# Kernel optimization log

Hardware: AMD Instinct MI355X
Metric: run time of the kernel (lower is better)

Reference implementation:

```python
import jax, jax.numpy as jnp
import numpy as np

N, E, G = 20000, 600000, 128
NF, HID, L, H = 16, 128, 4, 4
C = HID // H  # 32 per-head out dim
BN_EPS = 1e-5


def setup_inputs() -> dict:
    key = jax.random.key(0)
    ks = jax.random.split(key, 24)
    inp = {}
    inp['x'] = jax.random.normal(ks[0], (N, NF), dtype=jnp.float32)
    inp['edge_index'] = jax.random.randint(ks[1], (2, E), 0, N, dtype=jnp.int32)
    inp['batch'] = jnp.sort(jax.random.randint(ks[2], (N,), 0, G, dtype=jnp.int32))
    s = 0.05
    inp['emb_w'] = jax.random.normal(ks[3], (NF, HID), dtype=jnp.float32) * s
    inp['emb_b'] = jnp.zeros((HID,), dtype=jnp.float32)
    inp['gat_w'] = jax.random.normal(ks[4], (L, HID, HID), dtype=jnp.float32) * s
    inp['att_src'] = jax.random.normal(ks[5], (L, H, C), dtype=jnp.float32) * s
    inp['att_dst'] = jax.random.normal(ks[6], (L, H, C), dtype=jnp.float32) * s
    inp['gat_b'] = jnp.zeros((L, HID), dtype=jnp.float32)
    inp['bn_gamma'] = jnp.ones((L, HID), dtype=jnp.float32)
    inp['bn_beta'] = jnp.zeros((L, HID), dtype=jnp.float32)
    inp['bn_mean'] = jax.random.normal(ks[7], (L, HID), dtype=jnp.float32) * 0.01
    inp['bn_var'] = jnp.ones((L, HID), dtype=jnp.float32)
    inp['fc1_w'] = jax.random.normal(ks[8], (HID, 64), dtype=jnp.float32) * s
    inp['fc1_b'] = jnp.zeros((64,), dtype=jnp.float32)
    inp['fc2_w'] = jax.random.normal(ks[9], (64, 32), dtype=jnp.float32) * s
    inp['fc2_b'] = jnp.zeros((32,), dtype=jnp.float32)
    inp['bg_w'] = jax.random.normal(ks[10], (32, 1), dtype=jnp.float32) * s
    inp['bg_b'] = jnp.zeros((1,), dtype=jnp.float32)
    return inp


def _gat_layer(x, W, a_src, a_dst, bias, src, dst):
    # PyG GATConv (concat=True, negative_slope=0.2, self-loops already appended)
    h = (x @ W).reshape(N, H, C)                      # [N,H,C]
    s_src = jnp.sum(h * a_src, axis=-1)               # [N,H]
    s_dst = jnp.sum(h * a_dst, axis=-1)               # [N,H]
    e = jax.nn.leaky_relu(s_src[src] + s_dst[dst], 0.2)  # [E+N,H]
    m = jax.ops.segment_max(e, dst, num_segments=N)   # per-dest softmax max
    ex = jnp.exp(e - m[dst])
    denom = jax.ops.segment_sum(ex, dst, num_segments=N)
    alpha = ex / (denom[dst] + 1e-16)                 # [E+N,H]
    msg = h[src] * alpha[:, :, None]                  # [E+N,H,C]
    out = jax.ops.segment_sum(msg, dst, num_segments=N)
    return out.reshape(N, HID) + bias


def reference(x, edge_index, batch, emb_w, emb_b, gat_w, att_src, att_dst, gat_b,
              bn_gamma, bn_beta, bn_mean, bn_var, fc1_w, fc1_b, fc2_w, fc2_b, bg_w, bg_b):
    # add self loops (PyG GATConv default)
    loops = jnp.arange(N, dtype=edge_index.dtype)
    src = jnp.concatenate([edge_index[0], loops])
    dst = jnp.concatenate([edge_index[1], loops])

    h = jax.nn.relu(x @ emb_w + emb_b)
    for l in range(L):
        hn = _gat_layer(h, gat_w[l], att_src[l], att_dst[l], gat_b[l], src, dst)
        hn = (hn - bn_mean[l]) * (bn_gamma[l] / jnp.sqrt(bn_var[l] + BN_EPS)) + bn_beta[l]
        h = h + jax.nn.relu(hn)

    # global mean pool over graphs
    sums = jax.ops.segment_sum(h, batch, num_segments=G)
    cnts = jax.ops.segment_sum(jnp.ones((N,), dtype=h.dtype), batch, num_segments=G)
    g = sums / jnp.maximum(cnts, 1.0)[:, None]        # [G,HID]

    g = jax.nn.relu(g @ fc1_w + fc1_b)
    g = jax.nn.relu(g @ fc2_w + fc2_b)
    out = g @ bg_w + bg_b                              # band_gap head
    return out.squeeze(-1)                             # [G]
```

## Files before the change

kernel.cpp:

```cpp
#include <hip/hip_runtime.h>
#include <math.h>

#define HID 128
#define NF  16
#define NH  4
#define HC  32
#define NLAYERS 4

__global__ void k_init(int* __restrict__ counts, int N,
                       const float* __restrict__ gat_b, const float* __restrict__ gamma,
                       const float* __restrict__ beta, const float* __restrict__ mean,
                       const float* __restrict__ var,
                       float* __restrict__ scale, float* __restrict__ shift) {
    int i = blockIdx.x * blockDim.x + threadIdx.x;
    if (i < N) counts[i] = 1;
    if (i < NLAYERS * HID) {
        float sc = gamma[i] / sqrtf(var[i] + 1e-5f);
        scale[i] = sc;
        shift[i] = beta[i] + (gat_b[i] - mean[i]) * sc;
    }
}

__global__ void k_count_edges(const int* __restrict__ dst, int E, int* __restrict__ counts) {
    int i = blockIdx.x * blockDim.x + threadIdx.x;
    if (i < E) atomicAdd(&counts[dst[i]], 1);
}

__global__ __launch_bounds__(1024) void k_scan(const int* __restrict__ counts,
                                               int* __restrict__ row_ptr,
                                               int* __restrict__ col,
                                               int* __restrict__ fill, int N) {
    __shared__ int sums[1024];
    const int t = threadIdx.x;
    const int per = (N + 1023) >> 10;
    const int beg = min(t * per, N);
    const int end = min(beg + per, N);
    int s = 0;
    for (int i = beg; i < end; ++i) s += counts[i];
    sums[t] = s;
    __syncthreads();
    for (int off = 1; off < 1024; off <<= 1) {
        int v = (t >= off) ? sums[t - off] : 0;
        __syncthreads();
        sums[t] += v;
        __syncthreads();
    }
    int run = sums[t] - s;
    for (int i = beg; i < end; ++i) {
        row_ptr[i] = run;
        col[run] = i;
        fill[i] = 1;
        run += counts[i];
    }
    if (t == 1023) row_ptr[N] = sums[1023];
}

__global__ void k_scatter(const int* __restrict__ src, const int* __restrict__ dst, int E,
                          const int* __restrict__ row_ptr, int* __restrict__ fill,
                          int* __restrict__ col) {
    int i = blockIdx.x * blockDim.x + threadIdx.x;
    if (i < E) {
        int d = dst[i];
        int pos = atomicAdd(&fill[d], 1);
        col[row_ptr[d] + pos] = src[i];
    }
}

__global__ __launch_bounds__(256) void k_embed(const float* __restrict__ x,
                                               const float* __restrict__ w,
                                               const float* __restrict__ b,
                                               float* __restrict__ h, int N) {
    __shared__ float ws_[NF * HID];
    __shared__ float bs[HID];
    const int t = threadIdx.x;
    for (int i = t; i < NF * HID; i += 256) ws_[i] = w[i];
    if (t < HID) bs[t] = b[t];
    __syncthreads();
    const int n = blockIdx.x * 2 + (t >> 7);
    const int j = t & 127;
    if (n >= N) return;
    float a = bs[j];
    const float4* xp = (const float4*)(x + (size_t)n * NF);
#pragma unroll
    for (int q = 0; q < 4; ++q) {
        const float4 xv = xp[q];
        a = fmaf(xv.x, ws_[(q * 4 + 0) * HID + j], a);
        a = fmaf(xv.y, ws_[(q * 4 + 1) * HID + j], a);
        a = fmaf(xv.z, ws_[(q * 4 + 2) * HID + j], a);
        a = fmaf(xv.w, ws_[(q * 4 + 3) * HID + j], a);
    }
    h[(size_t)n * HID + j] = fmaxf(a, 0.f);
}

__global__ __launch_bounds__(256) void k_gemm_attn(
    const float* __restrict__ h, const float* __restrict__ W,
    const float* __restrict__ a_src, const float* __restrict__ a_dst,
    float* __restrict__ hproj, float* __restrict__ ssrc, float* __restrict__ sdst, int N) {
    __shared__ float As[2][16][68];
    __shared__ float Bs[2][16][132];
    const int tid = threadIdx.x;
    const int m0 = blockIdx.x * 64;
    const int tx = tid & 15;
    const int ty = tid >> 4;
    float acc[4][8];
#pragma unroll
    for (int i = 0; i < 4; ++i)
#pragma unroll
        for (int j = 0; j < 8; ++j) acc[i][j] = 0.f;

    const int arow = tid >> 2;
    const int ak   = (tid & 3) << 2;
    const int brow = tid >> 4;
    const int bcol = (tid & 15) << 3;
    const int gr = m0 + arow;
    const float* aptr = h + (size_t)gr * HID + ak;
    const float* bptr = W + brow * HID + bcol;

    float4 av = (gr < N) ? *(const float4*)aptr : make_float4(0.f, 0.f, 0.f, 0.f);
    float4 bv0 = *(const float4*)bptr;
    float4 bv1 = *(const float4*)(bptr + 4);
    As[0][ak + 0][arow] = av.x; As[0][ak + 1][arow] = av.y;
    As[0][ak + 2][arow] = av.z; As[0][ak + 3][arow] = av.w;
    *(float4*)&Bs[0][brow][bcol] = bv0;
    *(float4*)&Bs[0][brow][bcol + 4] = bv1;
    __syncthreads();

    for (int k0 = 0; k0 < 8; ++k0) {
        const int cur = k0 & 1, nxt = cur ^ 1;
        if (k0 < 7) {
            av = (gr < N) ? *(const float4*)(aptr + (k0 + 1) * 16)
                          : make_float4(0.f, 0.f, 0.f, 0.f);
            bv0 = *(const float4*)(bptr + (size_t)(k0 + 1) * 16 * HID);
            bv1 = *(const float4*)(bptr + (size_t)(k0 + 1) * 16 * HID + 4);
        }
#pragma unroll
        for (int k = 0; k < 16; ++k) {
            const float4 a  = *(const float4*)&As[cur][k][ty << 2];
            const float4 b0 = *(const float4*)&Bs[cur][k][tx << 3];
            const float4 b1 = *(const float4*)&Bs[cur][k][(tx << 3) + 4];
            const float aa[4] = {a.x, a.y, a.z, a.w};
            const float bb[8] = {b0.x, b0.y, b0.z, b0.w, b1.x, b1.y, b1.z, b1.w};
#pragma unroll
            for (int i = 0; i < 4; ++i)
#pragma unroll
                for (int j = 0; j < 8; ++j) acc[i][j] = fmaf(aa[i], bb[j], acc[i][j]);
        }
        if (k0 < 7) {
            As[nxt][ak + 0][arow] = av.x; As[nxt][ak + 1][arow] = av.y;
            As[nxt][ak + 2][arow] = av.z; As[nxt][ak + 3][arow] = av.w;
            *(float4*)&Bs[nxt][brow][bcol] = bv0;
            *(float4*)&Bs[nxt][brow][bcol + 4] = bv1;
        }
        __syncthreads();
    }

    const int head = tx >> 2;
    float asv[8], adv[8];
#pragma unroll
    for (int j = 0; j < 8; ++j) {
        asv[j] = a_src[head * HC + (tx & 3) * 8 + j];
        adv[j] = a_dst[head * HC + (tx & 3) * 8 + j];
    }
#pragma unroll
    for (int i = 0; i < 4; ++i) {
        const int r = m0 + (ty << 2) + i;
        if (r < N) {
            const float4 o0 = make_float4(acc[i][0], acc[i][1], acc[i][2], acc[i][3]);
            const float4 o1 = make_float4(acc[i][4], acc[i][5], acc[i][6], acc[i][7]);
            *(float4*)(hproj + (size_t)r * HID + (tx << 3)) = o0;
            *(float4*)(hproj + (size_t)r * HID + (tx << 3) + 4) = o1;
            float ps = 0.f, pd = 0.f;
#pragma unroll
            for (int j = 0; j < 8; ++j) {
                ps = fmaf(acc[i][j], asv[j], ps);
                pd = fmaf(acc[i][j], adv[j], pd);
            }
            ps += __shfl_xor(ps, 1); ps += __shfl_xor(ps, 2);
            pd += __shfl_xor(pd, 1); pd += __shfl_xor(pd, 2);
            if ((tx & 3) == 0) { ssrc[r * NH + head] = ps; sdst[r * NH + head] = pd; }
        }
    }
}

#define LEAKY(e) ((e) > 0.f ? (e) : 0.2f * (e))
__global__ __launch_bounds__(256) void k_sagg(
    float* __restrict__ h, const float4* __restrict__ hproj4,
    const float4* __restrict__ ssrc4, const float4* __restrict__ sdst4,
    const int* __restrict__ row_ptr, const int* __restrict__ col,
    const float4* __restrict__ scale4, const float4* __restrict__ shift4, int N) {
    __shared__ int   s_col[4][64];
    __shared__ float s_alpha[4][256];
    const int t = threadIdx.x;
    const int w = t >> 6;
    const int lane = t & 63;
    const int n = blockIdx.x * 4 + w;
    if (n >= N) return;
    const int beg = row_ptr[n], end = row_ptr[n + 1];
    const float4 sd = sdst4[n];

    const int i0 = beg + lane;
    const bool v0 = i0 < end;
    int sn0 = 0;
    float fe0 = -1e30f, fe1 = -1e30f, fe2 = -1e30f, fe3 = -1e30f;
    float M0 = -1e30f, M1 = -1e30f, M2 = -1e30f, M3 = -1e30f;
    if (v0) {
        sn0 = col[i0];
        const float4 ss = ssrc4[sn0];
        fe0 = LEAKY(ss.x + sd.x); fe1 = LEAKY(ss.y + sd.y);
        fe2 = LEAKY(ss.z + sd.z); fe3 = LEAKY(ss.w + sd.w);
        M0 = fe0; M1 = fe1; M2 = fe2; M3 = fe3;
    }
    for (int i = i0 + 64; i < end; i += 64) {
        const float4 ss = ssrc4[col[i]];
        M0 = fmaxf(M0, LEAKY(ss.x + sd.x));
        M1 = fmaxf(M1, LEAKY(ss.y + sd.y));
        M2 = fmaxf(M2, LEAKY(ss.z + sd.z));
        M3 = fmaxf(M3, LEAKY(ss.w + sd.w));
    }
#pragma unroll
    for (int o = 32; o >= 1; o >>= 1) {
        M0 = fmaxf(M0, __shfl_xor(M0, o));
        M1 = fmaxf(M1, __shfl_xor(M1, o));
        M2 = fmaxf(M2, __shfl_xor(M2, o));
        M3 = fmaxf(M3, __shfl_xor(M3, o));
    }
    float S0 = 0.f, S1 = 0.f, S2 = 0.f, S3 = 0.f;
    float t0 = 0.f, t1 = 0.f, t2 = 0.f, t3 = 0.f;
    if (v0) {
        t0 = __expf(fe0 - M0); t1 = __expf(fe1 - M1);
        t2 = __expf(fe2 - M2); t3 = __expf(fe3 - M3);
        S0 = t0; S1 = t1; S2 = t2; S3 = t3;
    }
    for (int i = i0 + 64; i < end; i += 64) {
        const float4 ss = ssrc4[col[i]];
        S0 += __expf(LEAKY(ss.x + sd.x) - M0);
        S1 += __expf(LEAKY(ss.y + sd.y) - M1);
        S2 += __expf(LEAKY(ss.z + sd.z) - M2);
        S3 += __expf(LEAKY(ss.w + sd.w) - M3);
    }
#pragma unroll
    for (int o = 32; o >= 1; o >>= 1) {
        S0 += __shfl_xor(S0, o);
        S1 += __shfl_xor(S1, o);
        S2 += __shfl_xor(S2, o);
        S3 += __shfl_xor(S3, o);
    }
    const float inv0 = 1.f / (S0 + 1e-16f);
    const float inv1 = 1.f / (S1 + 1e-16f);
    const float inv2 = 1.f / (S2 + 1e-16f);
    const float inv3 = 1.f / (S3 + 1e-16f);

    const int c  = lane & 31;
    const int hh = c >> 3;
    const int eh = lane >> 5;
    float4 acc = make_float4(0.f, 0.f, 0.f, 0.f);
    {
        if (v0) {
            s_col[w][lane] = sn0;
            float4 a;
            a.x = t0 * inv0; a.y = t1 * inv1; a.z = t2 * inv2; a.w = t3 * inv3;
            *(float4*)&s_alpha[w][lane << 2] = a;
        }
        asm volatile("s_waitcnt lgkmcnt(0)" ::: "memory");
        const int cnt = min(64, end - beg);
#pragma unroll 4
        for (int j2 = 0; j2 < cnt; j2 += 2) {
            const int j = j2 + eh;
            float a = 0.f; int sn = s_col[w][0];
            if (j < cnt) { sn = s_col[w][j]; a = s_alpha[w][(j << 2) | hh]; }
            const float4 hv = hproj4[(size_t)sn * 32 + c];
            acc.x = fmaf(a, hv.x, acc.x);
            acc.y = fmaf(a, hv.y, acc.y);
            acc.z = fmaf(a, hv.z, acc.z);
            acc.w = fmaf(a, hv.w, acc.w);
        }
    }
    for (int c0 = beg + 64; c0 < end; c0 += 64) {
        const int i = c0 + lane;
        if (i < end) {
            const int sn = col[i];
            const float4 ss = ssrc4[sn];
            float4 a;
            a.x = __expf(LEAKY(ss.x + sd.x) - M0) * inv0;
            a.y = __expf(LEAKY(ss.y + sd.y) - M1) * inv1;
            a.z = __expf(LEAKY(ss.z + sd.z) - M2) * inv2;
            a.w = __expf(LEAKY(ss.w + sd.w) - M3) * inv3;
            s_col[w][lane] = sn;
            *(float4*)&s_alpha[w][lane << 2] = a;
        }
        asm volatile("s_waitcnt lgkmcnt(0)" ::: "memory");
        const int cnt = min(64, end - c0);
#pragma unroll 4
        for (int j2 = 0; j2 < cnt; j2 += 2) {
            const int j = j2 + eh;
            float a = 0.f; int sn = s_col[w][0];
            if (j < cnt) { sn = s_col[w][j]; a = s_alpha[w][(j << 2) | hh]; }
            const float4 hv = hproj4[(size_t)sn * 32 + c];
            acc.x = fmaf(a, hv.x, acc.x);
            acc.y = fmaf(a, hv.y, acc.y);
            acc.z = fmaf(a, hv.z, acc.z);
            acc.w = fmaf(a, hv.w, acc.w);
        }
    }
    acc.x += __shfl_xor(acc.x, 32);
    acc.y += __shfl_xor(acc.y, 32);
    acc.z += __shfl_xor(acc.z, 32);
    acc.w += __shfl_xor(acc.w, 32);

    if (lane < 32) {
        const float4 sc = scale4[c];
        const float4 sh = shift4[c];
        float4* hp = (float4*)h + (size_t)n * 32 + c;
        float4 hv = *hp;
        hv.x += fmaxf(fmaf(acc.x, sc.x, sh.x), 0.f);
        hv.y += fmaxf(fmaf(acc.y, sc.y, sh.y), 0.f);
        hv.z += fmaxf(fmaf(acc.z, sc.z, sh.z), 0.f);
        hv.w += fmaxf(fmaf(acc.w, sc.w, sh.w), 0.f);
        *hp = hv;
    }
}

__global__ __launch_bounds__(256) void k_poolhead(
    const float4* __restrict__ h4, const int* __restrict__ batch,
    const float* __restrict__ w1, const float* __restrict__ b1,
    const float* __restrict__ w2, const float* __restrict__ b2,
    const float* __restrict__ w3, const float* __restrict__ b3,
    float* __restrict__ out, int N) {
    __shared__ float4 red[8][32];
    __shared__ float gp[HID];
    __shared__ float l1[64];
    __shared__ float l2[32];
    const int g = blockIdx.x;
    const int t = threadIdx.x;
    const int c4 = t & 31, r = t >> 5;
    int lo = 0, hi = N;
    while (lo < hi) { int mid = (lo + hi) >> 1; if (batch[mid] < g) lo = mid + 1; else hi = mid; }
    int lo2 = lo, hi2 = N;
    while (lo2 < hi2) { int mid = (lo2 + hi2) >> 1; if (batch[mid] < g + 1) lo2 = mid + 1; else hi2 = mid; }
    float4 acc = make_float4(0.f, 0.f, 0.f, 0.f);
    for (int i = lo + r; i < lo2; i += 8) {
        const float4 v = h4[(size_t)i * 32 + c4];
        acc.x += v.x; acc.y += v.y; acc.z += v.z; acc.w += v.w;
    }
    red[r][c4] = acc;
    __syncthreads();
    if (r == 0) {
#pragma unroll
        for (int k = 1; k < 8; ++k) {
            const float4 v = red[k][c4];
            acc.x += v.x; acc.y += v.y; acc.z += v.z; acc.w += v.w;
        }
        const float invc = 1.f / fmaxf((float)(lo2 - lo), 1.f);
        float4 o = make_float4(acc.x * invc, acc.y * invc, acc.z * invc, acc.w * invc);
        *(float4*)&gp[c4 << 2] = o;
    }
    __syncthreads();
    if (t < 64) {
        float a = b1[t];
        for (int k = 0; k < HID; ++k) a = fmaf(gp[k], w1[k * 64 + t], a);
        l1[t] = fmaxf(a, 0.f);
    }
    __syncthreads();
    if (t < 32) {
        float a2 = b2[t];
        for (int k = 0; k < 64; ++k) a2 = fmaf(l1[k], w2[k * 32 + t], a2);
        l2[t] = fmaxf(a2, 0.f);
    }
    __syncthreads();
    if (t == 0) {
        float a3 = b3[0];
        for (int k = 0; k < 32; ++k) a3 = fmaf(l2[k], w3[k], a3);
        out[g] = a3;
    }
}

extern "C" void kernel_launch(void* const* d_in, const int* in_sizes, int n_in,
                              void* d_out, int out_size, void* d_ws, size_t ws_size,
                              hipStream_t stream) {
    const float* x        = (const float*)d_in[0];
    const int*   eidx     = (const int*)d_in[1];
    const int*   batch    = (const int*)d_in[2];
    const float* emb_w    = (const float*)d_in[3];
    const float* emb_b    = (const float*)d_in[4];
    const float* gat_w    = (const float*)d_in[5];
    const float* att_src  = (const float*)d_in[6];
    const float* att_dst  = (const float*)d_in[7];
    const float* gat_b    = (const float*)d_in[8];
    const float* bn_gamma = (const float*)d_in[9];
    const float* bn_beta  = (const float*)d_in[10];
    const float* bn_mean  = (const float*)d_in[11];
    const float* bn_var   = (const float*)d_in[12];
    const float* fc1_w    = (const float*)d_in[13];
    const float* fc1_b    = (const float*)d_in[14];
    const float* fc2_w    = (const float*)d_in[15];
    const float* fc2_b    = (const float*)d_in[16];
    const float* bg_w     = (const float*)d_in[17];
    const float* bg_b     = (const float*)d_in[18];
    float* out = (float*)d_out;

    const int N = in_sizes[0] / NF;
    const int E = in_sizes[1] / 2;
    const int G = out_size;

    const int* esrc = eidx;
    const int* edst = eidx + E;

    char* ws = (char*)d_ws;
    size_t off = 0;
    auto alloc = [&](size_t bytes) -> void* {
        void* p = ws + off;
        off += (bytes + 255) & ~(size_t)255;
        return p;
    };
    float*  h       = (float*)alloc((size_t)N * HID * sizeof(float));
    float*  hproj   = (float*)alloc((size_t)N * HID * sizeof(float));
    float*  ssrc    = (float*)alloc((size_t)N * NH * sizeof(float));
    float*  sdst    = (float*)alloc((size_t)N * NH * sizeof(float));
    float*  bnscale = (float*)alloc((size_t)NLAYERS * HID * sizeof(float));
    float*  bnshift = (float*)alloc((size_t)NLAYERS * HID * sizeof(float));
    int*    row_ptr = (int*)alloc((size_t)(N + 1) * sizeof(int));
    int*    counts  = (int*)alloc((size_t)N * sizeof(int));
    int*    col     = (int*)alloc((size_t)(E + N) * sizeof(int));
    (void)ws_size; (void)n_in;

    const int TB = 256;
    k_init<<<(N + TB - 1) / TB, TB, 0, stream>>>(counts, N, gat_b, bn_gamma, bn_beta,
                                                 bn_mean, bn_var, bnscale, bnshift);
    k_count_edges<<<(E + TB - 1) / TB, TB, 0, stream>>>(edst, E, counts);
    k_scan<<<1, 1024, 0, stream>>>(counts, row_ptr, col, counts, N);
    k_scatter<<<(E + TB - 1) / TB, TB, 0, stream>>>(esrc, edst, E, row_ptr, counts, col);

    k_embed<<<(N + 1) / 2, 256, 0, stream>>>(x, emb_w, emb_b, h, N);

    for (int l = 0; l < NLAYERS; ++l) {
        k_gemm_attn<<<(N + 63) / 64, 256, 0, stream>>>(
            h, gat_w + (size_t)l * HID * HID,
            att_src + (size_t)l * NH * HC, att_dst + (size_t)l * NH * HC,
            hproj, ssrc, sdst, N);
        k_sagg<<<(N + 3) / 4, 256, 0, stream>>>(
            h, (const float4*)hproj, (const float4*)ssrc, (const float4*)sdst,
            row_ptr, col,
            (const float4*)(bnscale + l * HID), (const float4*)(bnshift + l * HID), N);
    }

    k_poolhead<<<G, 256, 0, stream>>>((const float4*)h, batch,
                                      fc1_w, fc1_b, fc2_w, fc2_b, bg_w, bg_b, out, N);
}
```

Measured before the change: 390.8 us.

## Replace single-block CSR scan with three-kernel multi-block parallel scan

Replaces the single 1024-thread block prefix scan over per-node edge counts, where each thread serially walks about 20 nodes, with a three-phase scan: per-block reductions, a single small block scanning the partial sums, and a per-block final scan that writes row_ptr, col self-loops and fill. This spreads the CSR construction scan across many CUs instead of one. It adds two extra kernel launches, and k_scanp only handles up to 128 blocks (N up to 32768), which silently breaks for larger N.

```diff
diff --git a/kernel.cpp b/kernel.cpp
--- a/kernel.cpp
+++ b/kernel.cpp
@@ -6,6 +6,7 @@
 #define NH  4
 #define HC  32
 #define NLAYERS 4
+#define SCAN_B 256
 
 __global__ void k_init(int* __restrict__ counts, int N,
                        const float* __restrict__ gat_b, const float* __restrict__ gamma,
@@ -26,33 +27,63 @@
     if (i < E) atomicAdd(&counts[dst[i]], 1);
 }
 
-__global__ __launch_bounds__(1024) void k_scan(const int* __restrict__ counts,
-                                               int* __restrict__ row_ptr,
-                                               int* __restrict__ col,
-                                               int* __restrict__ fill, int N) {
-    __shared__ int sums[1024];
-    const int t = threadIdx.x;
-    const int per = (N + 1023) >> 10;
-    const int beg = min(t * per, N);
-    const int end = min(beg + per, N);
-    int s = 0;
-    for (int i = beg; i < end; ++i) s += counts[i];
-    sums[t] = s;
-    __syncthreads();
-    for (int off = 1; off < 1024; off <<= 1) {
-        int v = (t >= off) ? sums[t - off] : 0;
-        __syncthreads();
-        sums[t] += v;
-        __syncthreads();
-    }
-    int run = sums[t] - s;
-    for (int i = beg; i < end; ++i) {
-        row_ptr[i] = run;
-        col[run] = i;
+__global__ __launch_bounds__(SCAN_B) void k_partial(const int* __restrict__ counts,
+                                                    int* __restrict__ partials, int N) {
+    __shared__ int s[SCAN_B];
+    const int t = threadIdx.x;
+    const int i = blockIdx.x * SCAN_B + t;
+    int v = (i < N) ? counts[i] : 0;
+    s[t] = v;
+    __syncthreads();
+#pragma unroll
+    for (int off = SCAN_B / 2; off >= 1; off >>= 1) {
+        if (t < off) s[t] += s[t + off];
+        __syncthreads();
+    }
+    if (t == 0) partials[blockIdx.x] = s[0];
+}
+
+__global__ __launch_bounds__(128) void k_scanp(const int* __restrict__ partials,
+                                               int* __restrict__ bases,
+                                               int* __restrict__ row_ptr_N, int B) {
+    __shared__ int s[128];
+    const int t = threadIdx.x;
+    int v = (t < B) ? partials[t] : 0;
+    s[t] = v;
+    __syncthreads();
+    for (int off = 1; off < 128; off <<= 1) {
+        int u = (t >= off) ? s[t - off] : 0;
+        __syncthreads();
+        s[t] += u;
+        __syncthreads();
+    }
+    if (t < B) bases[t] = s[t] - v;
+    if (t == 127) *row_ptr_N = s[127];
+}
+
+__global__ __launch_bounds__(SCAN_B) void k_final(const int* __restrict__ counts,
+                                                  const int* __restrict__ bases,
+                                                  int* __restrict__ row_ptr,
+                                                  int* __restrict__ col,
+                                                  int* __restrict__ fill, int N) {
+    __shared__ int s[SCAN_B];
+    const int t = threadIdx.x;
+    const int i = blockIdx.x * SCAN_B + t;
+    const int v = (i < N) ? counts[i] : 0;
+    s[t] = v;
+    __syncthreads();
+    for (int off = 1; off < SCAN_B; off <<= 1) {
+        int u = (t >= off) ? s[t - off] : 0;
+        __syncthreads();
+        s[t] += u;
+        __syncthreads();
+    }
+    if (i < N) {
+        const int row = bases[blockIdx.x] + s[t] - v;
+        row_ptr[i] = row;
+        col[row] = i;
         fill[i] = 1;
-        run += counts[i];
-    }
-    if (t == 1023) row_ptr[N] = sums[1023];
+    }
 }
 
 __global__ void k_scatter(const int* __restrict__ src, const int* __restrict__ dst, int E,
@@ -412,22 +443,28 @@
         off += (bytes + 255) & ~(size_t)255;
         return p;
     };
-    float*  h       = (float*)alloc((size_t)N * HID * sizeof(float));
-    float*  hproj   = (float*)alloc((size_t)N * HID * sizeof(float));
-    float*  ssrc    = (float*)alloc((size_t)N * NH * sizeof(float));
-    float*  sdst    = (float*)alloc((size_t)N * NH * sizeof(float));
-    float*  bnscale = (float*)alloc((size_t)NLAYERS * HID * sizeof(float));
-    float*  bnshift = (float*)alloc((size_t)NLAYERS * HID * sizeof(float));
-    int*    row_ptr = (int*)alloc((size_t)(N + 1) * sizeof(int));
-    int*    counts  = (int*)alloc((size_t)N * sizeof(int));
-    int*    col     = (int*)alloc((size_t)(E + N) * sizeof(int));
+    float*  h        = (float*)alloc((size_t)N * HID * sizeof(float));
+    float*  hproj    = (float*)alloc((size_t)N * HID * sizeof(float));
+    float*  ssrc     = (float*)alloc((size_t)N * NH * sizeof(float));
+    float*  sdst     = (float*)alloc((size_t)N * NH * sizeof(float));
+    float*  bnscale  = (float*)alloc((size_t)NLAYERS * HID * sizeof(float));
+    float*  bnshift  = (float*)alloc((size_t)NLAYERS * HID * sizeof(float));
+    int*    row_ptr  = (int*)alloc((size_t)(N + 1) * sizeof(int));
+    int*    counts   = (int*)alloc((size_t)N * sizeof(int));
+    int*    col      = (int*)alloc((size_t)(E + N) * sizeof(int));
+    int*    partials = (int*)alloc(1024 * sizeof(int));
+    int*    bases    = (int*)alloc(1024 * sizeof(int));
     (void)ws_size; (void)n_in;
 
     const int TB = 256;
+    const int NB = (N + SCAN_B - 1) / SCAN_B;
+
     k_init<<<(N + TB - 1) / TB, TB, 0, stream>>>(counts, N, gat_b, bn_gamma, bn_beta,
                                                  bn_mean, bn_var, bnscale, bnshift);
     k_count_edges<<<(E + TB - 1) / TB, TB, 0, stream>>>(edst, E, counts);
-    k_scan<<<1, 1024, 0, stream>>>(counts, row_ptr, col, counts, N);
+    k_partial<<<NB, SCAN_B, 0, stream>>>(counts, partials, N);
+    k_scanp<<<1, 128, 0, stream>>>(partials, bases, row_ptr + N, NB);
+    k_final<<<NB, SCAN_B, 0, stream>>>(counts, bases, row_ptr, col, counts, N);
     k_scatter<<<(E + TB - 1) / TB, TB, 0, stream>>>(esrc, edst, E, row_ptr, counts, col);
 
     k_embed<<<(N + 1) / 2, 256, 0, stream>>>(x, emb_w, emb_b, h, N);
```

Result: faster. 354.7 us (-9.2%).
